# Performance work log

Hardware: AMD Instinct MI355X
Metric: run time of the kernel (lower is better)

## Reference

```python
import jax, jax.numpy as jnp
import numpy as np

B, Q, K, C, H = 4, 1024, 1024, 1024, 16
L = C            # latent_dim (== in_dim per module construction)
CH = L // H      # head_dim = 64


def _ln(x, w, b):
    m = jnp.mean(x, -1, keepdims=True)
    v = jnp.mean((x - m) ** 2, -1, keepdims=True)
    return (x - m) * jax.lax.rsqrt(v + 1e-5) * w + b


def setup_inputs() -> dict:
    key = jax.random.key(0)
    ks = jax.random.split(key, 16)
    s = 0.02
    return {
        "queries": jax.random.normal(ks[0], (B, Q, C), jnp.float32),
        "contexts": jax.random.normal(ks[1], (B, K, C), jnp.float32),
        "queries_hidden": jax.random.normal(ks[2], (B, Q, L), jnp.float32),
        "sa_norm_w": jnp.ones((C,), jnp.float32),
        "sa_norm_b": jnp.zeros((C,), jnp.float32),
        "sa_qkv_w": jax.random.normal(ks[3], (C, 2 * L + C), jnp.float32) * s,
        "sa_out_w": jax.random.normal(ks[4], (C, C), jnp.float32) * s,
        "sa_out_b": jnp.zeros((C,), jnp.float32),
        "ca_norm_w": jnp.ones((C,), jnp.float32),
        "ca_norm_b": jnp.zeros((C,), jnp.float32),
        "gru_w_ih": jax.random.normal(ks[5], (3 * L, C), jnp.float32) * s,
        "gru_w_hh": jax.random.normal(ks[6], (3 * L, L), jnp.float32) * s,
        "gru_b_ih": jnp.zeros((3 * L,), jnp.float32),
        "gru_b_hh": jnp.zeros((3 * L,), jnp.float32),
        "ca_k_w": jax.random.normal(ks[7], (C, L), jnp.float32) * s,
        "ca_v_w": jax.random.normal(ks[8], (C, C), jnp.float32) * s,
        "ca_out_w": jax.random.normal(ks[9], (C, C), jnp.float32) * s,
        "ca_out_b": jnp.zeros((C,), jnp.float32),
        "ln1_w": jnp.ones((C,), jnp.float32),
        "ln1_b": jnp.zeros((C,), jnp.float32),
        "lin1_w": jax.random.normal(ks[10], (C, 2 * C), jnp.float32) * s,
        "ln2_w": jnp.ones((2 * C,), jnp.float32),
        "ln2_b": jnp.zeros((2 * C,), jnp.float32),
        "lin2_w": jax.random.normal(ks[11], (2 * C, C), jnp.float32) * s,
    }


def reference(queries, contexts, queries_hidden,
              sa_norm_w, sa_norm_b, sa_qkv_w, sa_out_w, sa_out_b,
              ca_norm_w, ca_norm_b, gru_w_ih, gru_w_hh, gru_b_ih, gru_b_hh,
              ca_k_w, ca_v_w, ca_out_w, ca_out_b,
              ln1_w, ln1_b, lin1_w, ln2_w, ln2_b, lin2_w):
    scale = 1.0 / jnp.sqrt(jnp.asarray(C, queries.dtype))

    # ---- SelfAttention (pre-norm, residual) ----
    xn = _ln(queries, sa_norm_w, sa_norm_b)
    qkv = (xn @ sa_qkv_w).reshape(B, Q, H, -1)          # [B,Q,H, 2*CH + C/H]
    q, k, v = jnp.split(qkv, [CH, 2 * CH], axis=-1)
    e = jnp.einsum('nqhc,nkhc->nhqk', q, k) * scale
    a = jax.nn.softmax(e, axis=-1)
    o = jnp.einsum('nhqk,nkhc->nqhc', a, v).reshape(B, Q, C)
    x = o @ sa_out_w + sa_out_b + queries

    # ---- AttentionDynamicQuery (GRU-updated queries, cross-attn) ----
    x_pre = x
    xn = _ln(x, ca_norm_w, ca_norm_b)
    xf = xn.reshape(B * Q, C)
    hf = queries_hidden.reshape(B * Q, L)
    gi = xf @ gru_w_ih.T + gru_b_ih                     # [BQ, 3L]
    gh = hf @ gru_w_hh.T + gru_b_hh
    gir, giz, gin = jnp.split(gi, 3, axis=-1)
    ghr, ghz, ghn = jnp.split(gh, 3, axis=-1)
    r = jax.nn.sigmoid(gir + ghr)
    z = jax.nn.sigmoid(giz + ghz)
    n = jnp.tanh(gin + r * ghn)
    h = (1.0 - z) * n + z * hf                          # PyTorch GRUCell update
    qh = h.reshape(B, Q, H, CH)                         # new queries_hidden

    kk = (contexts @ ca_k_w).reshape(B, K, H, CH)
    vv = (contexts @ ca_v_w).reshape(B, K, H, C // H)
    energy = jnp.einsum('nqhc,nkhc->nhqk', qh, kk)      # returned UNscaled
    att = jax.nn.softmax(energy * scale, axis=-1)
    o = jnp.einsum('nhqk,nkhc->nqhc', att, vv).reshape(B, Q, C)
    x = o @ ca_out_w + ca_out_b + x_pre

    # ---- MLP: LN -> SiLU -> Linear -> LN -> SiLU -> Linear, residual ----
    m = jax.nn.silu(_ln(x, ln1_w, ln1_b)) @ lin1_w
    m = jax.nn.silu(_ln(m, ln2_w, ln2_b)) @ lin2_w
    out = x + m                                         # dropout(p=0) = identity
    return (out, energy, qh)
```

## Files before the change

### kernel.cpp

```cpp
#include <hip/hip_runtime.h>
#include <hip/hip_bf16.h>
#include <math.h>

static constexpr float SCALE = 0.03125f;

typedef __attribute__((ext_vector_type(4))) float f32x4;
typedef __attribute__((ext_vector_type(8))) __bf16 bf16x8;
typedef __attribute__((ext_vector_type(4))) __bf16 bf16x4;

__device__ __forceinline__ void g2l16(const void* g, void* l) {
  __builtin_amdgcn_global_load_lds(
      (const __attribute__((address_space(1))) unsigned int*)g,
      (__attribute__((address_space(3))) unsigned int*)l,
      16, 0, 0);
}

__global__ __launch_bounds__(256) void prep_all(
    const float* __restrict__ sa_qkv_w, const float* __restrict__ ca_k_w,
    const float* __restrict__ ca_v_w, const float* __restrict__ sa_out_w,
    const float* __restrict__ ca_out_w, const float* __restrict__ lin1_w,
    const float* __restrict__ lin2_w, const float* __restrict__ gru_w_ih,
    const float* __restrict__ gru_w_hh, const float* __restrict__ qhid,
    const float* __restrict__ contexts,
    const float* __restrict__ queries, const float* __restrict__ sa_norm_w,
    const float* __restrict__ sa_norm_b,
    __bf16* __restrict__ qkvT, __bf16* __restrict__ kT, __bf16* __restrict__ vT,
    __bf16* __restrict__ saoT, __bf16* __restrict__ caoT, __bf16* __restrict__ lin1T,
    __bf16* __restrict__ lin2T, __bf16* __restrict__ ihB, __bf16* __restrict__ hhB,
    __bf16* __restrict__ qhB, __bf16* __restrict__ ctxB, __bf16* __restrict__ xnB) {
  int bid = blockIdx.x;
  int t = threadIdx.x;
  if (bid >= 9984) {
    int row = bid - 9984;
    int c = t * 4;
    float4 v = *(const float4*)(queries + (size_t)row * 1024 + c);
    float s = v.x + v.y + v.z + v.w;
    float s2 = v.x*v.x + v.y*v.y + v.z*v.z + v.w*v.w;
    #pragma unroll
    for (int off = 32; off > 0; off >>= 1) {
      s += __shfl_xor(s, off);
      s2 += __shfl_xor(s2, off);
    }
    __shared__ float red[4], red2[4];
    int wv = t >> 6;
    if ((t & 63) == 0) { red[wv] = s; red2[wv] = s2; }
    __syncthreads();
    float S  = red[0] + red[1] + red[2] + red[3];
    float S2 = red2[0] + red2[1] + red2[2] + red2[3];
    float mean = S / 1024.f;
    float var = S2 / 1024.f - mean * mean;
    float rs = rsqrtf(var + 1e-5f);
    float vv[4] = {v.x, v.y, v.z, v.w};
    bf16x4 o;
    #pragma unroll
    for (int j = 0; j < 4; ++j)
      o[j] = (__bf16)((vv[j] - mean) * rs * sa_norm_w[c+j] + sa_norm_b[c+j]);
    *(bf16x4*)(xnB + (size_t)row * 1024 + c) = o;
    return;
  }
  if (bid >= 2816) {
    const float* csrc; __bf16* cdst; int cbase;
    if (bid < 4352)      { csrc = gru_w_ih; cdst = ihB;  cbase = 2816; }
    else if (bid < 5888) { csrc = gru_w_hh; cdst = hhB;  cbase = 4352; }
    else if (bid < 7936) { csrc = qhid;     cdst = qhB;  cbase = 5888; }
    else                 { csrc = contexts; cdst = ctxB; cbase = 7936; }
    size_t idx = ((size_t)(bid - cbase) * 256 + t) * 8;
    float4 a = *(const float4*)(csrc + idx);
    float4 b = *(const float4*)(csrc + idx + 4);
    bf16x8 o = {(__bf16)a.x,(__bf16)a.y,(__bf16)a.z,(__bf16)a.w,
                (__bf16)b.x,(__bf16)b.y,(__bf16)b.z,(__bf16)b.w};
    *(bf16x8*)(cdst + idx) = o;
    return;
  }
  const float* src; __bf16* dst; int Kd, N, base;
  if (bid < 768)       { src = sa_qkv_w; dst = qkvT;  Kd = 1024; N = 3072; base = 0; }
  else if (bid < 1024) { src = ca_k_w;   dst = kT;    Kd = 1024; N = 1024; base = 768; }
  else if (bid < 1280) { src = ca_v_w;   dst = vT;    Kd = 1024; N = 1024; base = 1024; }
  else if (bid < 1536) { src = sa_out_w; dst = saoT;  Kd = 1024; N = 1024; base = 1280; }
  else if (bid < 1792) { src = ca_out_w; dst = caoT;  Kd = 1024; N = 1024; base = 1536; }
  else if (bid < 2304) { src = lin1_w;   dst = lin1T; Kd = 1024; N = 2048; base = 1792; }
  else                 { src = lin2_w;   dst = lin2T; Kd = 2048; N = 1024; base = 2304; }
  int tid = bid - base;
  int ntx = N >> 6;
  int n0 = (tid % ntx) * 64, k0 = (tid / ntx) * 64;
  __shared__ float tile[64][65];
  #pragma unroll
  for (int i = 0; i < 16; ++i) {
    int idx = i * 256 + t; int r = idx >> 6, c = idx & 63;
    tile[r][c] = src[(size_t)(k0 + r) * N + n0 + c];
  }
  __syncthreads();
  #pragma unroll
  for (int i = 0; i < 16; ++i) {
    int idx = i * 256 + t; int r = idx >> 6, c = idx & 63;
    dst[(size_t)(n0 + r) * Kd + k0 + c] = (__bf16)tile[c][r];
  }
}

template <int NV>
__global__ __launch_bounds__(256) void ln_bf16(
    const float* __restrict__ xf, const __bf16* __restrict__ xb,
    const float* __restrict__ w, const float* __restrict__ b,
    __bf16* __restrict__ out, int silu) {
  const int D = NV * 1024;
  int row = blockIdx.x, t = threadIdx.x;
  float vals[NV * 4];
  float s = 0.f, s2 = 0.f;
  #pragma unroll
  for (int i = 0; i < NV; ++i) {
    int c = (i * 256 + t) * 4;
    float4 v;
    if (xf) {
      v = *(const float4*)(xf + (size_t)row * D + c);
    } else {
      bf16x4 vb = *(const bf16x4*)(xb + (size_t)row * D + c);
      v = make_float4((float)vb[0], (float)vb[1], (float)vb[2], (float)vb[3]);
    }
    vals[i*4+0] = v.x; vals[i*4+1] = v.y; vals[i*4+2] = v.z; vals[i*4+3] = v.w;
    s += v.x + v.y + v.z + v.w;
    s2 += v.x*v.x + v.y*v.y + v.z*v.z + v.w*v.w;
  }
  #pragma unroll
  for (int off = 32; off > 0; off >>= 1) {
    s += __shfl_xor(s, off);
    s2 += __shfl_xor(s2, off);
  }
  __shared__ float red[4], red2[4];
  int wv = t >> 6;
  if ((t & 63) == 0) { red[wv] = s; red2[wv] = s2; }
  __syncthreads();
  float S  = red[0] + red[1] + red[2] + red[3];
  float S2 = red2[0] + red2[1] + red2[2] + red2[3];
  float mean = S / D;
  float var = S2 / D - mean * mean;
  float rs = rsqrtf(var + 1e-5f);
  #pragma unroll
  for (int i = 0; i < NV; ++i) {
    int c = (i * 256 + t) * 4;
    bf16x4 o;
    #pragma unroll
    for (int j = 0; j < 4; ++j) {
      float v = (vals[i*4+j] - mean) * rs * w[c+j] + b[c+j];
      if (silu) v = v / (1.f + __expf(-v));
      o[j] = (__bf16)v;
    }
    *(bf16x4*)(out + (size_t)row * D + c) = o;
  }
}

__device__ __forceinline__ void gemm_body(
    const __bf16* __restrict__ A, long long lda,
    const __bf16* __restrict__ B, long long ldb,
    float* __restrict__ outF, __bf16* __restrict__ outB, long long ldc,
    const float* __restrict__ bias, const float* __restrict__ res,
    int K, int bm, int bn, __bf16* __restrict__ VTout, int vmode) {
  __shared__ __bf16 Asm0[8192];
  __shared__ __bf16 Bsm0[8192];
  __shared__ __bf16 Asm1[8192];
  __shared__ __bf16 Bsm1[8192];
  int t = threadIdx.x;
  int lane = t & 63, w = t >> 6;
  int l15 = lane & 15, kg = lane >> 4;
  int wm = (w >> 1) * 64, wn = (w & 1) * 64;

  f32x4 acc[4][4];
  #pragma unroll
  for (int i = 0; i < 4; ++i)
    #pragma unroll
    for (int j = 0; j < 4; ++j) acc[i][j] = (f32x4)(0.0f);

  const __bf16* ga[4]; const __bf16* gb[4];
  int lo[4];
  #pragma unroll
  for (int i = 0; i < 4; ++i) {
    int slot = i * 256 + t;
    int row = slot >> 3, s = slot & 7;
    int sx = s ^ (row & 7);
    ga[i] = A + (size_t)(bm + row) * lda + (sx << 3);
    gb[i] = B + (size_t)(bn + row) * ldb + (sx << 3);
    lo[i] = (i * 256 + w * 64) << 3;
  }

  auto STAGE = [&](__bf16* As, __bf16* Bs, int k0) {
    #pragma unroll
    for (int i = 0; i < 4; ++i) g2l16(ga[i] + k0, As + lo[i]);
    #pragma unroll
    for (int i = 0; i < 4; ++i) g2l16(gb[i] + k0, Bs + lo[i]);
  };
  auto COMPUTE = [&](const __bf16* As, const __bf16* Bs) {
    #pragma unroll
    for (int kk = 0; kk < 2; ++kk) {
      bf16x8 af[4], bfr[4];
      #pragma unroll
      for (int mi = 0; mi < 4; ++mi) {
        int row = wm + mi * 16 + l15;
        int ks = kk * 4 + kg;
        af[mi] = *(const bf16x8*)(As + row * 64 + ((ks ^ (row & 7)) << 3));
      }
      #pragma unroll
      for (int ni = 0; ni < 4; ++ni) {
        int row = wn + ni * 16 + l15;
        int ks = kk * 4 + kg;
        bfr[ni] = *(const bf16x8*)(Bs + row * 64 + ((ks ^ (row & 7)) << 3));
      }
      #pragma unroll
      for (int mi = 0; mi < 4; ++mi)
        #pragma unroll
        for (int ni = 0; ni < 4; ++ni)
          acc[mi][ni] = __builtin_amdgcn_mfma_f32_16x16x32_bf16(
              af[mi], bfr[ni], acc[mi][ni], 0, 0, 0);
    }
  };
  #define GEMM_SYNC() do { \
    asm volatile("s_waitcnt vmcnt(0)" ::: "memory"); \
    __builtin_amdgcn_s_barrier(); \
    __builtin_amdgcn_sched_barrier(0); \
  } while (0)

  STAGE(Asm0, Bsm0, 0);
  GEMM_SYNC();
  int nk = K >> 6;
  for (int kt = 0; kt + 2 < nk; kt += 2) {
    STAGE(Asm1, Bsm1, (kt + 1) << 6);
    COMPUTE(Asm0, Bsm0);
    GEMM_SYNC();
    STAGE(Asm0, Bsm0, (kt + 2) << 6);
    COMPUTE(Asm1, Bsm1);
    GEMM_SYNC();
  }
  STAGE(Asm1, Bsm1, (nk - 1) << 6);
  COMPUTE(Asm0, Bsm0);
  GEMM_SYNC();
  COMPUTE(Asm1, Bsm1);
  #undef GEMM_SYNC

  int cw = bn + wn;
  int isV = 0;
  if (vmode == 1)      isV = (cw % 192) == 128;
  else if (vmode == 2) isV = cw >= 1024;

  if (isV) {
    int h = (vmode == 1) ? (cw / 192) : ((cw - 1024) >> 6);
    int rowb = bm + wm;
    int b = rowb >> 10, k0 = rowb & 1023;
    __bf16* scr = (w < 2 ? Asm0 : Bsm0) + (w & 1) * 4096;
    #pragma unroll
    for (int mi = 0; mi < 4; ++mi) {
      #pragma unroll
      for (int ni = 0; ni < 4; ++ni) {
        int d = ni * 16 + l15;
        int sw = (d & 7) << 3;
        #pragma unroll
        for (int r = 0; r < 4; ++r) {
          int kl = mi * 16 + kg * 4 + r;
          scr[d * 64 + (kl ^ sw)] = (__bf16)acc[mi][ni][r];
        }
      }
    }
    #pragma unroll
    for (int i = 0; i < 8; ++i) {
      int idx = i * 64 + lane;
      int d = idx >> 3, kc = (idx & 7) * 8;
      bf16x8 v = *(const bf16x8*)&scr[d * 64 + (kc ^ ((d & 7) << 3))];
      *(bf16x8*)(VTout + ((size_t)((b * 16 + h) * 64 + d) << 10) + k0 + kc) = v;
    }
    return;
  }

  #pragma unroll
  for (int mi = 0; mi < 4; ++mi) {
    #pragma unroll
    for (int ni = 0; ni < 4; ++ni) {
      int rbase = bm + wm + mi * 16 + kg * 4;
      int c = bn + wn + ni * 16 + l15;
      #pragma unroll
      for (int r = 0; r < 4; ++r) {
        float val = acc[mi][ni][r];
        if (bias) val += bias[c];
        size_t off = (size_t)(rbase + r) * ldc + c;
        if (res) val += res[off];
        if (outF) outF[off] = val;
        if (outB) outB[off] = (__bf16)val;
      }
    }
  }
}

__global__ __launch_bounds__(256) void gemm_bf16(
    const __bf16* __restrict__ A, long long lda,
    const __bf16* __restrict__ B, long long ldb,
    float* __restrict__ outF, __bf16* __restrict__ outB, long long ldc,
    const float* __restrict__ bias, const float* __restrict__ res, int K,
    __bf16* __restrict__ VTout, int vmode) {
  int nwg = gridDim.x * gridDim.y;
  int orig = blockIdx.y * gridDim.x + blockIdx.x;
  int swz = (orig & 7) * (nwg >> 3) + (orig >> 3);
  gemm_body(A, lda, B, ldb, outF, outB, ldc, bias, res, K,
            (swz / gridDim.x) * 128, (swz % gridDim.x) * 128, VTout, vmode);
}

__global__ __launch_bounds__(256) void gemm_dual(
    const __bf16* __restrict__ A0, long long lda0, const __bf16* __restrict__ B0, long long ldb0,
    float* __restrict__ oF0, __bf16* __restrict__ oB0, long long ldc0,
    const float* __restrict__ bias0, const float* __restrict__ res0, int K0, int gx0, int nb0,
    const __bf16* __restrict__ A1, long long lda1, const __bf16* __restrict__ B1, long long ldb1,
    float* __restrict__ oF1, __bf16* __restrict__ oB1, long long ldc1,
    const float* __restrict__ bias1, const float* __restrict__ res1, int K1, int gx1,
    __bf16* __restrict__ VT1, int vm1) {
  int bid = blockIdx.x;
  if (bid < nb0) {
    int swz = (bid & 7) * (nb0 >> 3) + (bid >> 3);
    gemm_body(A0, lda0, B0, ldb0, oF0, oB0, ldc0, bias0, res0, K0,
              (swz / gx0) * 128, (swz % gx0) * 128, nullptr, 0);
  } else {
    int b = bid - nb0;
    int nb1 = gridDim.x - nb0;
    int swz = (b & 7) * (nb1 >> 3) + (b >> 3);
    gemm_body(A1, lda1, B1, ldb1, oF1, oB1, ldc1, bias1, res1, K1,
              (swz / gx1) * 128, (swz % gx1) * 128, VT1, vm1);
  }
}

__global__ __launch_bounds__(256) void gru_kernel(
    const __bf16* __restrict__ gi, const __bf16* __restrict__ gh,
    const float* __restrict__ hf, float* __restrict__ qh, __bf16* __restrict__ qhb) {
  size_t e0 = ((size_t)blockIdx.x * 256 + threadIdx.x) * 8;
  int row = (int)(e0 >> 10), col = (int)(e0 & 1023);
  size_t base = (size_t)row * 3072 + col;
  bf16x8 vir = *(const bf16x8*)(gi + base);
  bf16x8 viz = *(const bf16x8*)(gi + base + 1024);
  bf16x8 vin = *(const bf16x8*)(gi + base + 2048);
  bf16x8 vhr = *(const bf16x8*)(gh + base);
  bf16x8 vhz = *(const bf16x8*)(gh + base + 1024);
  bf16x8 vhn = *(const bf16x8*)(gh + base + 2048);
  float4 h0 = *(const float4*)(hf + e0);
  float4 h1 = *(const float4*)(hf + e0 + 4);
  float hv[8] = {h0.x, h0.y, h0.z, h0.w, h1.x, h1.y, h1.z, h1.w};
  float q[8];
  #pragma unroll
  for (int j = 0; j < 8; ++j) {
    float r = 1.f / (1.f + __expf(-((float)vir[j] + (float)vhr[j])));
    float z = 1.f / (1.f + __expf(-((float)viz[j] + (float)vhz[j])));
    float n = tanhf((float)vin[j] + r * (float)vhn[j]);
    q[j] = (1.f - z) * n + z * hv[j];
  }
  *(float4*)(qh + e0)     = make_float4(q[0], q[1], q[2], q[3]);
  *(float4*)(qh + e0 + 4) = make_float4(q[4], q[5], q[6], q[7]);
  bf16x8 qb;
  #pragma unroll
  for (int j = 0; j < 8; ++j) qb[j] = (__bf16)q[j];
  *(bf16x8*)(qhb + e0) = qb;
}

template <int E>
__global__ __launch_bounds__(256) void flash_attn(
    const __bf16* __restrict__ Qb, long long q_sb, long long q_sh, int q_sm,
    const __bf16* __restrict__ Kb, long long k_sb, long long k_sh, int k_sm,
    const __bf16* __restrict__ VT, __bf16* __restrict__ Ob,
    float* __restrict__ energyOut, float scale) {
  __shared__ __bf16 Ksm[3][4096];
  __shared__ __bf16 Vsm[3][4096];
  __shared__ __bf16 Psm[128 * 64];
  __shared__ float corr_l[128];
  __shared__ float l_l[128];
  int g = blockIdx.y, b = g >> 4, h = g & 15;
  int qt = blockIdx.x * 128;
  const __bf16* Qg = Qb + (size_t)b * q_sb + (size_t)h * q_sh;
  const __bf16* Kg = Kb + (size_t)b * k_sb + (size_t)h * k_sh;
  const __bf16* Vg = VT + (size_t)g * 65536;
  int t = threadIdx.x, lane = t & 63, w = t >> 6;
  int l15 = lane & 15, kg = lane >> 4;
  int wq = w * 32;

  bf16x8 qf[2][2];
  #pragma unroll
  for (int nq = 0; nq < 2; ++nq)
    #pragma unroll
    for (int kk = 0; kk < 2; ++kk)
      qf[nq][kk] = *(const bf16x8*)(
          Qg + (size_t)(qt + wq + nq * 16 + l15) * q_sm + kk * 32 + kg * 8);

  f32x4 acc_o[2][4];
  #pragma unroll
  for (int i = 0; i < 2; ++i)
    #pragma unroll
    for (int j = 0; j < 4; ++j) acc_o[i][j] = (f32x4)(0.0f);
  float m_run[2] = {-1e30f, -1e30f};
  float l_run[2] = {0.f, 0.f};

  const __bf16* gK[2]; const __bf16* gV[2];
  int lo[2];
  #pragma unroll
  for (int i = 0; i < 2; ++i) {
    int slot = i * 256 + t;
    int row = slot >> 3, s = slot & 7, sx = s ^ (row & 7);
    gK[i] = Kg + (size_t)row * k_sm + (sx << 3);
    gV[i] = Vg + (size_t)row * 1024 + (sx << 3);
    lo[i] = (i * 256 + w * 64) << 3;
  }

  #pragma unroll
  for (int i = 0; i < 2; ++i) g2l16(gK[i], &Ksm[0][lo[i]]);
  #pragma unroll
  for (int i = 0; i < 2; ++i) g2l16(gV[i], &Vsm[0][lo[i]]);
  #pragma unroll
  for (int i = 0; i < 2; ++i) g2l16(gK[i] + (size_t)64 * k_sm, &Ksm[1][lo[i]]);
  #pragma unroll
  for (int i = 0; i < 2; ++i) g2l16(gV[i] + 64, &Vsm[1][lo[i]]);

  int rb = 0;
  for (int kvt = 0; kvt < 16; ++kvt) {
    if (E) {
      if (kvt == 0)       asm volatile("s_waitcnt vmcnt(4)" ::: "memory");
      else if (kvt == 1)  asm volatile("s_waitcnt vmcnt(12)" ::: "memory");
      else if (kvt == 15) asm volatile("s_waitcnt vmcnt(16)" ::: "memory");
      else                asm volatile("s_waitcnt vmcnt(20)" ::: "memory");
    } else {
      if (kvt == 15)      asm volatile("s_waitcnt vmcnt(0)" ::: "memory");
      else                asm volatile("s_waitcnt vmcnt(4)" ::: "memory");
    }
    __builtin_amdgcn_s_barrier();
    __builtin_amdgcn_sched_barrier(0);

    if (kvt < 14) {
      int sbuf = rb >= 1 ? rb - 1 : rb + 2;
      size_t ko = (size_t)(kvt + 2) << 6;
      #pragma unroll
      for (int i = 0; i < 2; ++i) g2l16(gK[i] + ko * k_sm, &Ksm[sbuf][lo[i]]);
      #pragma unroll
      for (int i = 0; i < 2; ++i) g2l16(gV[i] + ko, &Vsm[sbuf][lo[i]]);
    }
    const __bf16* Ks = Ksm[rb];
    const __bf16* Vs = Vsm[rb];

    f32x4 accs[4][2];
    #pragma unroll
    for (int i = 0; i < 4; ++i)
      #pragma unroll
      for (int j = 0; j < 2; ++j) accs[i][j] = (f32x4)(0.0f);
    __builtin_amdgcn_s_setprio(1);
    #pragma unroll
    for (int tt = 0; tt < 4; ++tt) {
      bf16x8 kf[2];
      #pragma unroll
      for (int kk = 0; kk < 2; ++kk) {
        int row = tt * 16 + l15;
        int ks = kk * 4 + kg;
        kf[kk] = *(const bf16x8*)(Ks + row * 64 + ((ks ^ (row & 7)) << 3));
      }
      #pragma unroll
      for (int nq = 0; nq < 2; ++nq)
        #pragma unroll
        for (int kk = 0; kk < 2; ++kk)
          accs[tt][nq] = __builtin_amdgcn_mfma_f32_16x16x32_bf16(
              kf[kk], qf[nq][kk], accs[tt][nq], 0, 0, 0);
    }
    __builtin_amdgcn_s_setprio(0);

    if (E) {
      int kv0 = kvt << 6;
      float* eg = energyOut + ((size_t)g << 20);
      #pragma unroll
      for (int nq = 0; nq < 2; ++nq) {
        int q = qt + wq + nq * 16 + l15;
        #pragma unroll
        for (int tt = 0; tt < 4; ++tt)
          __builtin_nontemporal_store(
              accs[tt][nq], (f32x4*)(eg + (size_t)q * 1024 + kv0 + tt * 16 + kg * 4));
      }
    }

    #pragma unroll
    for (int nq = 0; nq < 2; ++nq) {
      float tmax = -1e30f;
      #pragma unroll
      for (int tt = 0; tt < 4; ++tt)
        #pragma unroll
        for (int r = 0; r < 4; ++r) tmax = fmaxf(tmax, accs[tt][nq][r]);
      tmax *= scale;
      tmax = fmaxf(tmax, __shfl_xor(tmax, 16));
      tmax = fmaxf(tmax, __shfl_xor(tmax, 32));
      float m_new = fmaxf(m_run[nq], tmax);
      float corr = __expf(m_run[nq] - m_new);
      m_run[nq] = m_new;
      int q = wq + nq * 16 + l15;
      float psum = 0.f;
      #pragma unroll
      for (int tt = 0; tt < 4; ++tt) {
        bf16x4 p4;
        #pragma unroll
        for (int r = 0; r < 4; ++r) {
          float p = __expf(accs[tt][nq][r] * scale - m_new);
          psum += p;
          p4[r] = (__bf16)p;
        }
        int kvs = (tt * 16 + kg * 4) ^ ((q & 7) << 3);
        *(bf16x4*)(Psm + q * 64 + kvs) = p4;
      }
      psum += __shfl_xor(psum, 16);
      psum += __shfl_xor(psum, 32);
      l_run[nq] = l_run[nq] * corr + psum;
      if (kg == 0) corr_l[q] = corr;
    }

    #pragma unroll
    for (int mq = 0; mq < 2; ++mq) {
      f32x4 c4 = *(const f32x4*)&corr_l[wq + mq * 16 + kg * 4];
      #pragma unroll
      for (int nd = 0; nd < 4; ++nd)
        #pragma unroll
        for (int r = 0; r < 4; ++r) acc_o[mq][nd][r] *= c4[r];
    }
    __builtin_amdgcn_s_setprio(1);
    #pragma unroll
    for (int kk = 0; kk < 2; ++kk) {
      bf16x8 pf[2], vf[4];
      #pragma unroll
      for (int mq = 0; mq < 2; ++mq) {
        int row = wq + mq * 16 + l15;
        int kvs = (kk * 32 + kg * 8) ^ ((row & 7) << 3);
        pf[mq] = *(const bf16x8*)(Psm + row * 64 + kvs);
      }
      #pragma unroll
      for (int nd = 0; nd < 4; ++nd) {
        int vrow = nd * 16 + l15;
        vf[nd] = *(const bf16x8*)(Vs + vrow * 64 + (((kk * 4 + kg) ^ (vrow & 7)) << 3));
      }
      #pragma unroll
      for (int mq = 0; mq < 2; ++mq)
        #pragma unroll
        for (int nd = 0; nd < 4; ++nd)
          acc_o[mq][nd] = __builtin_amdgcn_mfma_f32_16x16x32_bf16(
              pf[mq], vf[nd], acc_o[mq][nd], 0, 0, 0);
    }
    __builtin_amdgcn_s_setprio(0);
    rb = rb == 2 ? 0 : rb + 1;
  }

  #pragma unroll
  for (int nq = 0; nq < 2; ++nq)
    if (kg == 0) l_l[wq + nq * 16 + l15] = l_run[nq];
  __syncthreads();

  #pragma unroll
  for (int mq = 0; mq < 2; ++mq) {
    f32x4 lv = *(const f32x4*)&l_l[wq + mq * 16 + kg * 4];
    #pragma unroll
    for (int nd = 0; nd < 4; ++nd) {
      int col = h * 64 + nd * 16 + l15;
      #pragma unroll
      for (int r = 0; r < 4; ++r) {
        int qrow = qt + wq + mq * 16 + kg * 4 + r;
        Ob[(size_t)(b * 1024 + qrow) * 1024 + col] = (__bf16)(acc_o[mq][nd][r] / lv[r]);
      }
    }
  }
}

extern "C" void kernel_launch(void* const* d_in, const int* in_sizes, int n_in,
                              void* d_out, int out_size, void* d_ws, size_t ws_size,
                              hipStream_t stream) {
  (void)in_sizes; (void)n_in; (void)out_size; (void)ws_size;
  const float* queries   = (const float*)d_in[0];
  const float* contexts  = (const float*)d_in[1];
  const float* qhid      = (const float*)d_in[2];
  const float* sa_norm_w = (const float*)d_in[3];
  const float* sa_norm_b = (const float*)d_in[4];
  const float* sa_qkv_w  = (const float*)d_in[5];
  const float* sa_out_w  = (const float*)d_in[6];
  const float* sa_out_b  = (const float*)d_in[7];
  const float* ca_norm_w = (const float*)d_in[8];
  const float* ca_norm_b = (const float*)d_in[9];
  const float* gru_w_ih  = (const float*)d_in[10];
  const float* gru_w_hh  = (const float*)d_in[11];
  const float* gru_b_ih  = (const float*)d_in[12];
  const float* gru_b_hh  = (const float*)d_in[13];
  const float* ca_k_w    = (const float*)d_in[14];
  const float* ca_v_w    = (const float*)d_in[15];
  const float* ca_out_w  = (const float*)d_in[16];
  const float* ca_out_b  = (const float*)d_in[17];
  const float* ln1_w     = (const float*)d_in[18];
  const float* ln1_b     = (const float*)d_in[19];
  const float* lin1_w    = (const float*)d_in[20];
  const float* ln2_w     = (const float*)d_in[21];
  const float* ln2_b     = (const float*)d_in[22];
  const float* lin2_w    = (const float*)d_in[23];

  float* out0   = (float*)d_out;
  float* energy = out0 + (size_t)4194304;
  float* qh_out = out0 + (size_t)71303168;

  const size_t MM = 1u << 20;
  float* ws = (float*)d_ws;
  float*  X     = ws;
  float*  X2    = ws + 4 * MM;
  __bf16* M1B    = (__bf16*)(ws + 9 * MM);
  __bf16* XN_b   = (__bf16*)(ws + 17 * MM);
  __bf16* QHID_b = (__bf16*)(ws + 19 * MM);
  __bf16* CTX_b  = (__bf16*)(ws + 21 * MM);
  __bf16* O_b    = (__bf16*)(ws + 23 * MM);
  __bf16* VT_b   = (__bf16*)(ws + 25 * MM);
  __bf16* QKV_b  = (__bf16*)(ws + 27 * MM);
  __bf16* KV_b   = (__bf16*)(ws + 27 * MM);
  __bf16* LN2_b  = (__bf16*)(ws);
  __bf16* qkvT   = (__bf16*)(ws + 33 * MM);
  __bf16* ihB    = (__bf16*)(ws + 34 * MM + MM / 2);
  __bf16* hhB    = (__bf16*)(ws + 36 * MM);
  __bf16* kT     = (__bf16*)(ws + 37 * MM + MM / 2);
  __bf16* vT     = (__bf16*)(ws + 38 * MM);
  __bf16* saoT   = (__bf16*)(ws + 38 * MM + MM / 2);
  __bf16* caoT   = (__bf16*)(ws + 39 * MM);
  __bf16* lin1T  = (__bf16*)(ws + 39 * MM + MM / 2);
  __bf16* lin2T  = (__bf16*)(ws + 40 * MM + MM / 2);
  __bf16* GI_b = (__bf16*)energy;
  __bf16* GH_b = (__bf16*)(energy + 6 * MM);

  const long long QKV_SB = 1024LL * 3072;
  const long long KV_SB  = 1024LL * 2048;

  prep_all<<<14080, 256, 0, stream>>>(
      sa_qkv_w, ca_k_w, ca_v_w, sa_out_w, ca_out_w, lin1_w, lin2_w,
      gru_w_ih, gru_w_hh, qhid, contexts, queries, sa_norm_w, sa_norm_b,
      qkvT, kT, vT, saoT, caoT, lin1T, lin2T, ihB, hhB, QHID_b, CTX_b, XN_b);

  gemm_bf16<<<dim3(24, 32), 256, 0, stream>>>(
      XN_b, 1024, qkvT, 1024, nullptr, QKV_b, 3072, nullptr, nullptr, 1024, VT_b, 1);
  flash_attn<0><<<dim3(8, 64), 256, 0, stream>>>(
      QKV_b, QKV_SB, 192, 3072, QKV_b + 64, QKV_SB, 192, 3072,
      VT_b, O_b, nullptr, SCALE);
  gemm_dual<<<1024, 256, 0, stream>>>(
      O_b, 1024, saoT, 1024, X, nullptr, 1024, sa_out_b, queries, 1024, 8, 256,
      QHID_b, 1024, hhB, 1024, nullptr, GH_b, 3072, gru_b_hh, nullptr, 1024, 24,
      nullptr, 0);

  ln_bf16<1><<<4096, 256, 0, stream>>>(X, nullptr, ca_norm_w, ca_norm_b, XN_b, 0);
  gemm_dual<<<1280, 256, 0, stream>>>(
      XN_b, 1024, ihB, 1024, nullptr, GI_b, 3072, gru_b_ih, nullptr, 1024, 24, 768,
      CTX_b, 1024, kT, 1024, nullptr, KV_b, 2048, nullptr, nullptr, 1024, 16,
      VT_b, 2);
  gru_kernel<<<2048, 256, 0, stream>>>(GI_b, GH_b, qhid, qh_out, QHID_b );

  flash_attn<1><<<dim3(8, 64), 256, 0, stream>>>(
      QHID_b, 1024LL * 1024, 64, 1024, KV_b, KV_SB, 64, 2048,
      VT_b, O_b, energy, SCALE);
  gemm_bf16<<<dim3(8, 32), 256, 0, stream>>>(
      O_b, 1024, caoT, 1024, X2, nullptr, 1024, ca_out_b, X, 1024, nullptr, 0);

  ln_bf16<1><<<4096, 256, 0, stream>>>(X2, nullptr, ln1_w, ln1_b, XN_b, 1);
  gemm_bf16<<<dim3(16, 32), 256, 0, stream>>>(
      XN_b, 1024, lin1T, 1024, nullptr, M1B, 2048, nullptr, nullptr, 1024, nullptr, 0);
  ln_bf16<2><<<4096, 256, 0, stream>>>(nullptr, M1B, ln2_w, ln2_b, LN2_b, 1);
  gemm_bf16<<<dim3(8, 32), 256, 0, stream>>>(
      LN2_b, 2048, lin2T, 2048, out0, nullptr, 1024, nullptr, X2, 2048, nullptr, 0);
}
```

Measured before the change: 609.5 us.

## Split prep into critical path and fuse remaining conversions into QKV GEMM launch

The prep work is split in two. A small kernel now transposes only the QKV weight and computes the first LayerNorm. The remaining weight transposes and bf16 casts run as extra blocks inside the same launch as the QKV projection GEMM, so that memory-bound conversion work can overlap with the compute-bound GEMM instead of preceding it. Shared memory is now a single buffer passed into gemm_body so it can be reused by the transpose tiles. The cost is that the merged launch uses the larger GEMM shared-memory footprint for every block, including the transpose blocks.

```diff
diff --git a/kernel.cpp b/kernel.cpp
--- a/kernel.cpp
+++ b/kernel.cpp
@@ -15,47 +15,310 @@
       16, 0, 0);
 }
 
-__global__ __launch_bounds__(256) void prep_all(
-    const float* __restrict__ sa_qkv_w, const float* __restrict__ ca_k_w,
-    const float* __restrict__ ca_v_w, const float* __restrict__ sa_out_w,
-    const float* __restrict__ ca_out_w, const float* __restrict__ lin1_w,
-    const float* __restrict__ lin2_w, const float* __restrict__ gru_w_ih,
-    const float* __restrict__ gru_w_hh, const float* __restrict__ qhid,
-    const float* __restrict__ contexts,
+__device__ __forceinline__ void wtrans_tile(
+    const float* __restrict__ src, __bf16* __restrict__ dst,
+    int Kd, int N, int tid, float (*tile)[65]) {
+  int t = threadIdx.x;
+  int ntx = N >> 6;
+  int n0 = (tid % ntx) * 64, k0 = (tid / ntx) * 64;
+  #pragma unroll
+  for (int i = 0; i < 16; ++i) {
+    int idx = i * 256 + t; int r = idx >> 6, c = idx & 63;
+    tile[r][c] = src[(size_t)(k0 + r) * N + n0 + c];
+  }
+  __syncthreads();
+  #pragma unroll
+  for (int i = 0; i < 16; ++i) {
+    int idx = i * 256 + t; int r = idx >> 6, c = idx & 63;
+    dst[(size_t)(n0 + r) * Kd + k0 + c] = (__bf16)tile[c][r];
+  }
+}
+
+__global__ __launch_bounds__(256) void prep_crit(
+    const float* __restrict__ sa_qkv_w,
     const float* __restrict__ queries, const float* __restrict__ sa_norm_w,
     const float* __restrict__ sa_norm_b,
-    __bf16* __restrict__ qkvT, __bf16* __restrict__ kT, __bf16* __restrict__ vT,
-    __bf16* __restrict__ saoT, __bf16* __restrict__ caoT, __bf16* __restrict__ lin1T,
-    __bf16* __restrict__ lin2T, __bf16* __restrict__ ihB, __bf16* __restrict__ hhB,
-    __bf16* __restrict__ qhB, __bf16* __restrict__ ctxB, __bf16* __restrict__ xnB) {
+    __bf16* __restrict__ qkvT, __bf16* __restrict__ xnB) {
   int bid = blockIdx.x;
   int t = threadIdx.x;
-  if (bid >= 9984) {
-    int row = bid - 9984;
-    int c = t * 4;
-    float4 v = *(const float4*)(queries + (size_t)row * 1024 + c);
-    float s = v.x + v.y + v.z + v.w;
-    float s2 = v.x*v.x + v.y*v.y + v.z*v.z + v.w*v.w;
-    #pragma unroll
-    for (int off = 32; off > 0; off >>= 1) {
-      s += __shfl_xor(s, off);
-      s2 += __shfl_xor(s2, off);
-    }
-    __shared__ float red[4], red2[4];
-    int wv = t >> 6;
-    if ((t & 63) == 0) { red[wv] = s; red2[wv] = s2; }
-    __syncthreads();
-    float S  = red[0] + red[1] + red[2] + red[3];
-    float S2 = red2[0] + red2[1] + red2[2] + red2[3];
-    float mean = S / 1024.f;
-    float var = S2 / 1024.f - mean * mean;
-    float rs = rsqrtf(var + 1e-5f);
-    float vv[4] = {v.x, v.y, v.z, v.w};
+  if (bid < 768) {
+    __shared__ float tile[64][65];
+    wtrans_tile(sa_qkv_w, qkvT, 1024, 3072, bid, tile);
+    return;
+  }
+  int row = bid - 768;
+  int c = t * 4;
+  float4 v = *(const float4*)(queries + (size_t)row * 1024 + c);
+  float s = v.x + v.y + v.z + v.w;
+  float s2 = v.x*v.x + v.y*v.y + v.z*v.z + v.w*v.w;
+  #pragma unroll
+  for (int off = 32; off > 0; off >>= 1) {
+    s += __shfl_xor(s, off);
+    s2 += __shfl_xor(s2, off);
+  }
+  __shared__ float red[4], red2[4];
+  int wv = t >> 6;
+  if ((t & 63) == 0) { red[wv] = s; red2[wv] = s2; }
+  __syncthreads();
+  float S  = red[0] + red[1] + red[2] + red[3];
+  float S2 = red2[0] + red2[1] + red2[2] + red2[3];
+  float mean = S / 1024.f;
+  float var = S2 / 1024.f - mean * mean;
+  float rs = rsqrtf(var + 1e-5f);
+  float vv[4] = {v.x, v.y, v.z, v.w};
+  bf16x4 o;
+  #pragma unroll
+  for (int j = 0; j < 4; ++j)
+    o[j] = (__bf16)((vv[j] - mean) * rs * sa_norm_w[c+j] + sa_norm_b[c+j]);
+  *(bf16x4*)(xnB + (size_t)row * 1024 + c) = o;
+}
+
+template <int NV>
+__global__ __launch_bounds__(256) void ln_bf16(
+    const float* __restrict__ xf, const __bf16* __restrict__ xb,
+    const float* __restrict__ w, const float* __restrict__ b,
+    __bf16* __restrict__ out, int silu) {
+  const int D = NV * 1024;
+  int row = blockIdx.x, t = threadIdx.x;
+  float vals[NV * 4];
+  float s = 0.f, s2 = 0.f;
+  #pragma unroll
+  for (int i = 0; i < NV; ++i) {
+    int c = (i * 256 + t) * 4;
+    float4 v;
+    if (xf) {
+      v = *(const float4*)(xf + (size_t)row * D + c);
+    } else {
+      bf16x4 vb = *(const bf16x4*)(xb + (size_t)row * D + c);
+      v = make_float4((float)vb[0], (float)vb[1], (float)vb[2], (float)vb[3]);
+    }
+    vals[i*4+0] = v.x; vals[i*4+1] = v.y; vals[i*4+2] = v.z; vals[i*4+3] = v.w;
+    s += v.x + v.y + v.z + v.w;
+    s2 += v.x*v.x + v.y*v.y + v.z*v.z + v.w*v.w;
+  }
+  #pragma unroll
+  for (int off = 32; off > 0; off >>= 1) {
+    s += __shfl_xor(s, off);
+    s2 += __shfl_xor(s2, off);
+  }
+  __shared__ float red[4], red2[4];
+  int wv = t >> 6;
+  if ((t & 63) == 0) { red[wv] = s; red2[wv] = s2; }
+  __syncthreads();
+  float S  = red[0] + red[1] + red[2] + red[3];
+  float S2 = red2[0] + red2[1] + red2[2] + red2[3];
+  float mean = S / D;
+  float var = S2 / D - mean * mean;
+  float rs = rsqrtf(var + 1e-5f);
+  #pragma unroll
+  for (int i = 0; i < NV; ++i) {
+    int c = (i * 256 + t) * 4;
     bf16x4 o;
     #pragma unroll
-    for (int j = 0; j < 4; ++j)
-      o[j] = (__bf16)((vv[j] - mean) * rs * sa_norm_w[c+j] + sa_norm_b[c+j]);
-    *(bf16x4*)(xnB + (size_t)row * 1024 + c) = o;
+    for (int j = 0; j < 4; ++j) {
+      float v = (vals[i*4+j] - mean) * rs * w[c+j] + b[c+j];
+      if (silu) v = v / (1.f + __expf(-v));
+      o[j] = (__bf16)v;
+    }
+    *(bf16x4*)(out + (size_t)row * D + c) = o;
+  }
+}
+
+__device__ __forceinline__ void gemm_body(
+    __bf16* __restrict__ sm,
+    const __bf16* __restrict__ A, long long lda,
+    const __bf16* __restrict__ B, long long ldb,
+    float* __restrict__ outF, __bf16* __restrict__ outB, long long ldc,
+    const float* __restrict__ bias, const float* __restrict__ res,
+    int K, int bm, int bn, __bf16* __restrict__ VTout, int vmode) {
+  __bf16* Asm0 = sm;
+  __bf16* Bsm0 = sm + 8192;
+  __bf16* Asm1 = sm + 16384;
+  __bf16* Bsm1 = sm + 24576;
+  int t = threadIdx.x;
+  int lane = t & 63, w = t >> 6;
+  int l15 = lane & 15, kg = lane >> 4;
+  int wm = (w >> 1) * 64, wn = (w & 1) * 64;
+
+  f32x4 acc[4][4];
+  #pragma unroll
+  for (int i = 0; i < 4; ++i)
+    #pragma unroll
+    for (int j = 0; j < 4; ++j) acc[i][j] = (f32x4)(0.0f);
+
+  const __bf16* ga[4]; const __bf16* gb[4];
+  int lo[4];
+  #pragma unroll
+  for (int i = 0; i < 4; ++i) {
+    int slot = i * 256 + t;
+    int row = slot >> 3, s = slot & 7;
+    int sx = s ^ (row & 7);
+    ga[i] = A + (size_t)(bm + row) * lda + (sx << 3);
+    gb[i] = B + (size_t)(bn + row) * ldb + (sx << 3);
+    lo[i] = (i * 256 + w * 64) << 3;
+  }
+
+  auto STAGE = [&](__bf16* As, __bf16* Bs, int k0) {
+    #pragma unroll
+    for (int i = 0; i < 4; ++i) g2l16(ga[i] + k0, As + lo[i]);
+    #pragma unroll
+    for (int i = 0; i < 4; ++i) g2l16(gb[i] + k0, Bs + lo[i]);
+  };
+  auto COMPUTE = [&](const __bf16* As, const __bf16* Bs) {
+    #pragma unroll
+    for (int kk = 0; kk < 2; ++kk) {
+      bf16x8 af[4], bfr[4];
+      #pragma unroll
+      for (int mi = 0; mi < 4; ++mi) {
+        int row = wm + mi * 16 + l15;
+        int ks = kk * 4 + kg;
+        af[mi] = *(const bf16x8*)(As + row * 64 + ((ks ^ (row & 7)) << 3));
+      }
+      #pragma unroll
+      for (int ni = 0; ni < 4; ++ni) {
+        int row = wn + ni * 16 + l15;
+        int ks = kk * 4 + kg;
+        bfr[ni] = *(const bf16x8*)(Bs + row * 64 + ((ks ^ (row & 7)) << 3));
+      }
+      #pragma unroll
+      for (int mi = 0; mi < 4; ++mi)
+        #pragma unroll
+        for (int ni = 0; ni < 4; ++ni)
+          acc[mi][ni] = __builtin_amdgcn_mfma_f32_16x16x32_bf16(
+              af[mi], bfr[ni], acc[mi][ni], 0, 0, 0);
+    }
+  };
+  #define GEMM_SYNC() do { \
+    asm volatile("s_waitcnt vmcnt(0)" ::: "memory"); \
+    __builtin_amdgcn_s_barrier(); \
+    __builtin_amdgcn_sched_barrier(0); \
+  } while (0)
+
+  STAGE(Asm0, Bsm0, 0);
+  GEMM_SYNC();
+  int nk = K >> 6;
+  for (int kt = 0; kt + 2 < nk; kt += 2) {
+    STAGE(Asm1, Bsm1, (kt + 1) << 6);
+    COMPUTE(Asm0, Bsm0);
+    GEMM_SYNC();
+    STAGE(Asm0, Bsm0, (kt + 2) << 6);
+    COMPUTE(Asm1, Bsm1);
+    GEMM_SYNC();
+  }
+  STAGE(Asm1, Bsm1, (nk - 1) << 6);
+  COMPUTE(Asm0, Bsm0);
+  GEMM_SYNC();
+  COMPUTE(Asm1, Bsm1);
+  #undef GEMM_SYNC
+
+  int cw = bn + wn;
+  int isV = 0;
+  if (vmode == 1)      isV = (cw % 192) == 128;
+  else if (vmode == 2) isV = cw >= 1024;
+
+  if (isV) {
+    int h = (vmode == 1) ? (cw / 192) : ((cw - 1024) >> 6);
+    int rowb = bm + wm;
+    int b = rowb >> 10, k0 = rowb & 1023;
+    __bf16* scr = (w < 2 ? Asm0 : Bsm0) + (w & 1) * 4096;
+    #pragma unroll
+    for (int mi = 0; mi < 4; ++mi) {
+      #pragma unroll
+      for (int ni = 0; ni < 4; ++ni) {
+        int d = ni * 16 + l15;
+        int sw = (d & 7) << 3;
+        #pragma unroll
+        for (int r = 0; r < 4; ++r) {
+          int kl = mi * 16 + kg * 4 + r;
+          scr[d * 64 + (kl ^ sw)] = (__bf16)acc[mi][ni][r];
+        }
+      }
+    }
+    #pragma unroll
+    for (int i = 0; i < 8; ++i) {
+      int idx = i * 64 + lane;
+      int d = idx >> 3, kc = (idx & 7) * 8;
+      bf16x8 v = *(const bf16x8*)&scr[d * 64 + (kc ^ ((d & 7) << 3))];
+      *(bf16x8*)(VTout + ((size_t)((b * 16 + h) * 64 + d) << 10) + k0 + kc) = v;
+    }
+    return;
+  }
+
+  #pragma unroll
+  for (int mi = 0; mi < 4; ++mi) {
+    #pragma unroll
+    for (int ni = 0; ni < 4; ++ni) {
+      int rbase = bm + wm + mi * 16 + kg * 4;
+      int c = bn + wn + ni * 16 + l15;
+      #pragma unroll
+      for (int r = 0; r < 4; ++r) {
+        float val = acc[mi][ni][r];
+        if (bias) val += bias[c];
+        size_t off = (size_t)(rbase + r) * ldc + c;
+        if (res) val += res[off];
+        if (outF) outF[off] = val;
+        if (outB) outB[off] = (__bf16)val;
+      }
+    }
+  }
+}
+
+__global__ __launch_bounds__(256) void gemm_bf16(
+    const __bf16* __restrict__ A, long long lda,
+    const __bf16* __restrict__ B, long long ldb,
+    float* __restrict__ outF, __bf16* __restrict__ outB, long long ldc,
+    const float* __restrict__ bias, const float* __restrict__ res, int K,
+    __bf16* __restrict__ VTout, int vmode) {
+  __shared__ __bf16 sm[32768];
+  int nwg = gridDim.x * gridDim.y;
+  int orig = blockIdx.y * gridDim.x + blockIdx.x;
+  int swz = (orig & 7) * (nwg >> 3) + (orig >> 3);
+  gemm_body(sm, A, lda, B, ldb, outF, outB, ldc, bias, res, K,
+            (swz / gridDim.x) * 128, (swz % gridDim.x) * 128, VTout, vmode);
+}
+
+__global__ __launch_bounds__(256) void gemm_dual(
+    const __bf16* __restrict__ A0, long long lda0, const __bf16* __restrict__ B0, long long ldb0,
+    float* __restrict__ oF0, __bf16* __restrict__ oB0, long long ldc0,
+    const float* __restrict__ bias0, const float* __restrict__ res0, int K0, int gx0, int nb0,
+    const __bf16* __restrict__ A1, long long lda1, const __bf16* __restrict__ B1, long long ldb1,
+    float* __restrict__ oF1, __bf16* __restrict__ oB1, long long ldc1,
+    const float* __restrict__ bias1, const float* __restrict__ res1, int K1, int gx1,
+    __bf16* __restrict__ VT1, int vm1) {
+  __shared__ __bf16 sm[32768];
+  int bid = blockIdx.x;
+  if (bid < nb0) {
+    int swz = (bid & 7) * (nb0 >> 3) + (bid >> 3);
+    gemm_body(sm, A0, lda0, B0, ldb0, oF0, oB0, ldc0, bias0, res0, K0,
+              (swz / gx0) * 128, (swz % gx0) * 128, nullptr, 0);
+  } else {
+    int b = bid - nb0;
+    int nb1 = gridDim.x - nb0;
+    int swz = (b & 7) * (nb1 >> 3) + (b >> 3);
+    gemm_body(sm, A1, lda1, B1, ldb1, oF1, oB1, ldc1, bias1, res1, K1,
+              (swz / gx1) * 128, (swz % gx1) * 128, VT1, vm1);
+  }
+}
+
+__global__ __launch_bounds__(256) void gemm_prep(
+    const __bf16* __restrict__ Aq, const __bf16* __restrict__ Bq,
+    __bf16* __restrict__ Cq, __bf16* __restrict__ VTq,
+    const float* __restrict__ ca_k_w, const float* __restrict__ ca_v_w,
+    const float* __restrict__ sa_out_w, const float* __restrict__ ca_out_w,
+    const float* __restrict__ lin1_w, const float* __restrict__ lin2_w,
+    const float* __restrict__ gru_w_ih, const float* __restrict__ gru_w_hh,
+    const float* __restrict__ qhid, const float* __restrict__ contexts,
+    __bf16* __restrict__ kT, __bf16* __restrict__ vT, __bf16* __restrict__ saoT,
+    __bf16* __restrict__ caoT, __bf16* __restrict__ lin1T, __bf16* __restrict__ lin2T,
+    __bf16* __restrict__ ihB, __bf16* __restrict__ hhB,
+    __bf16* __restrict__ qhB, __bf16* __restrict__ ctxB) {
+  __shared__ __bf16 sm[32768];
+  int bid = blockIdx.x;
+  int t = threadIdx.x;
+  if (bid < 768) {
+    int swz = (bid & 7) * 96 + (bid >> 3);
+    gemm_body(sm, Aq, 1024, Bq, 1024, nullptr, Cq, 3072, nullptr, nullptr, 1024,
+              (swz / 24) * 128, (swz % 24) * 128, VTq, 1);
     return;
   }
   if (bid >= 2816) {
@@ -73,252 +336,13 @@
     return;
   }
   const float* src; __bf16* dst; int Kd, N, base;
-  if (bid < 768)       { src = sa_qkv_w; dst = qkvT;  Kd = 1024; N = 3072; base = 0; }
-  else if (bid < 1024) { src = ca_k_w;   dst = kT;    Kd = 1024; N = 1024; base = 768; }
+  if (bid < 1024)      { src = ca_k_w;   dst = kT;    Kd = 1024; N = 1024; base = 768; }
   else if (bid < 1280) { src = ca_v_w;   dst = vT;    Kd = 1024; N = 1024; base = 1024; }
   else if (bid < 1536) { src = sa_out_w; dst = saoT;  Kd = 1024; N = 1024; base = 1280; }
   else if (bid < 1792) { src = ca_out_w; dst = caoT;  Kd = 1024; N = 1024; base = 1536; }
   else if (bid < 2304) { src = lin1_w;   dst = lin1T; Kd = 1024; N = 2048; base = 1792; }
   else                 { src = lin2_w;   dst = lin2T; Kd = 2048; N = 1024; base = 2304; }
-  int tid = bid - base;
-  int ntx = N >> 6;
-  int n0 = (tid % ntx) * 64, k0 = (tid / ntx) * 64;
-  __shared__ float tile[64][65];
-  #pragma unroll
-  for (int i = 0; i < 16; ++i) {
-    int idx = i * 256 + t; int r = idx >> 6, c = idx & 63;
-    tile[r][c] = src[(size_t)(k0 + r) * N + n0 + c];
-  }
-  __syncthreads();
-  #pragma unroll
-  for (int i = 0; i < 16; ++i) {
-    int idx = i * 256 + t; int r = idx >> 6, c = idx & 63;
-    dst[(size_t)(n0 + r) * Kd + k0 + c] = (__bf16)tile[c][r];
-  }
-}
-
-template <int NV>
-__global__ __launch_bounds__(256) void ln_bf16(
-    const float* __restrict__ xf, const __bf16* __restrict__ xb,
-    const float* __restrict__ w, const float* __restrict__ b,
-    __bf16* __restrict__ out, int silu) {
-  const int D = NV * 1024;
-  int row = blockIdx.x, t = threadIdx.x;
-  float vals[NV * 4];
-  float s = 0.f, s2 = 0.f;
-  #pragma unroll
-  for (int i = 0; i < NV; ++i) {
-    int c = (i * 256 + t) * 4;
-    float4 v;
-    if (xf) {
-      v = *(const float4*)(xf + (size_t)row * D + c);
-    } else {
-      bf16x4 vb = *(const bf16x4*)(xb + (size_t)row * D + c);
-      v = make_float4((float)vb[0], (float)vb[1], (float)vb[2], (float)vb[3]);
-    }
-    vals[i*4+0] = v.x; vals[i*4+1] = v.y; vals[i*4+2] = v.z; vals[i*4+3] = v.w;
-    s += v.x + v.y + v.z + v.w;
-    s2 += v.x*v.x + v.y*v.y + v.z*v.z + v.w*v.w;
-  }
-  #pragma unroll
-  for (int off = 32; off > 0; off >>= 1) {
-    s += __shfl_xor(s, off);
-    s2 += __shfl_xor(s2, off);
-  }
-  __shared__ float red[4], red2[4];
-  int wv = t >> 6;
-  if ((t & 63) == 0) { red[wv] = s; red2[wv] = s2; }
-  __syncthreads();
-  float S  = red[0] + red[1] + red[2] + red[3];
-  float S2 = red2[0] + red2[1] + red2[2] + red2[3];
-  float mean = S / D;
-  float var = S2 / D - mean * mean;
-  float rs = rsqrtf(var + 1e-5f);
-  #pragma unroll
-  for (int i = 0; i < NV; ++i) {
-    int c = (i * 256 + t) * 4;
-    bf16x4 o;
-    #pragma unroll
-    for (int j = 0; j < 4; ++j) {
-      float v = (vals[i*4+j] - mean) * rs * w[c+j] + b[c+j];
-      if (silu) v = v / (1.f + __expf(-v));
-      o[j] = (__bf16)v;
-    }
-    *(bf16x4*)(out + (size_t)row * D + c) = o;
-  }
-}
-
-__device__ __forceinline__ void gemm_body(
-    const __bf16* __restrict__ A, long long lda,
-    const __bf16* __restrict__ B, long long ldb,
-    float* __restrict__ outF, __bf16* __restrict__ outB, long long ldc,
-    const float* __restrict__ bias, const float* __restrict__ res,
-    int K, int bm, int bn, __bf16* __restrict__ VTout, int vmode) {
-  __shared__ __bf16 Asm0[8192];
-  __shared__ __bf16 Bsm0[8192];
-  __shared__ __bf16 Asm1[8192];
-  __shared__ __bf16 Bsm1[8192];
-  int t = threadIdx.x;
-  int lane = t & 63, w = t >> 6;
-  int l15 = lane & 15, kg = lane >> 4;
-  int wm = (w >> 1) * 64, wn = (w & 1) * 64;
-
-  f32x4 acc[4][4];
-  #pragma unroll
-  for (int i = 0; i < 4; ++i)
-    #pragma unroll
-    for (int j = 0; j < 4; ++j) acc[i][j] = (f32x4)(0.0f);
-
-  const __bf16* ga[4]; const __bf16* gb[4];
-  int lo[4];
-  #pragma unroll
-  for (int i = 0; i < 4; ++i) {
-    int slot = i * 256 + t;
-    int row = slot >> 3, s = slot & 7;
-    int sx = s ^ (row & 7);
-    ga[i] = A + (size_t)(bm + row) * lda + (sx << 3);
-    gb[i] = B + (size_t)(bn + row) * ldb + (sx << 3);
-    lo[i] = (i * 256 + w * 64) << 3;
-  }
-
-  auto STAGE = [&](__bf16* As, __bf16* Bs, int k0) {
-    #pragma unroll
-    for (int i = 0; i < 4; ++i) g2l16(ga[i] + k0, As + lo[i]);
-    #pragma unroll
-    for (int i = 0; i < 4; ++i) g2l16(gb[i] + k0, Bs + lo[i]);
-  };
-  auto COMPUTE = [&](const __bf16* As, const __bf16* Bs) {
-    #pragma unroll
-    for (int kk = 0; kk < 2; ++kk) {
-      bf16x8 af[4], bfr[4];
-      #pragma unroll
-      for (int mi = 0; mi < 4; ++mi) {
-        int row = wm + mi * 16 + l15;
-        int ks = kk * 4 + kg;
-        af[mi] = *(const bf16x8*)(As + row * 64 + ((ks ^ (row & 7)) << 3));
-      }
-      #pragma unroll
-      for (int ni = 0; ni < 4; ++ni) {
-        int row = wn + ni * 16 + l15;
-        int ks = kk * 4 + kg;
-        bfr[ni] = *(const bf16x8*)(Bs + row * 64 + ((ks ^ (row & 7)) << 3));
-      }
-      #pragma unroll
-      for (int mi = 0; mi < 4; ++mi)
-        #pragma unroll
-        for (int ni = 0; ni < 4; ++ni)
-          acc[mi][ni] = __builtin_amdgcn_mfma_f32_16x16x32_bf16(
-              af[mi], bfr[ni], acc[mi][ni], 0, 0, 0);
-    }
-  };
-  #define GEMM_SYNC() do { \
-    asm volatile("s_waitcnt vmcnt(0)" ::: "memory"); \
-    __builtin_amdgcn_s_barrier(); \
-    __builtin_amdgcn_sched_barrier(0); \
-  } while (0)
-
-  STAGE(Asm0, Bsm0, 0);
-  GEMM_SYNC();
-  int nk = K >> 6;
-  for (int kt = 0; kt + 2 < nk; kt += 2) {
-    STAGE(Asm1, Bsm1, (kt + 1) << 6);
-    COMPUTE(Asm0, Bsm0);
-    GEMM_SYNC();
-    STAGE(Asm0, Bsm0, (kt + 2) << 6);
-    COMPUTE(Asm1, Bsm1);
-    GEMM_SYNC();
-  }
-  STAGE(Asm1, Bsm1, (nk - 1) << 6);
-  COMPUTE(Asm0, Bsm0);
-  GEMM_SYNC();
-  COMPUTE(Asm1, Bsm1);
-  #undef GEMM_SYNC
-
-  int cw = bn + wn;
-  int isV = 0;
-  if (vmode == 1)      isV = (cw % 192) == 128;
-  else if (vmode == 2) isV = cw >= 1024;
-
-  if (isV) {
-    int h = (vmode == 1) ? (cw / 192) : ((cw - 1024) >> 6);
-    int rowb = bm + wm;
-    int b = rowb >> 10, k0 = rowb & 1023;
-    __bf16* scr = (w < 2 ? Asm0 : Bsm0) + (w & 1) * 4096;
-    #pragma unroll
-    for (int mi = 0; mi < 4; ++mi) {
-      #pragma unroll
-      for (int ni = 0; ni < 4; ++ni) {
-        int d = ni * 16 + l15;
-        int sw = (d & 7) << 3;
-        #pragma unroll
-        for (int r = 0; r < 4; ++r) {
-          int kl = mi * 16 + kg * 4 + r;
-          scr[d * 64 + (kl ^ sw)] = (__bf16)acc[mi][ni][r];
-        }
-      }
-    }
-    #pragma unroll
-    for (int i = 0; i < 8; ++i) {
-      int idx = i * 64 + lane;
-      int d = idx >> 3, kc = (idx & 7) * 8;
-      bf16x8 v = *(const bf16x8*)&scr[d * 64 + (kc ^ ((d & 7) << 3))];
-      *(bf16x8*)(VTout + ((size_t)((b * 16 + h) * 64 + d) << 10) + k0 + kc) = v;
-    }
-    return;
-  }
-
-  #pragma unroll
-  for (int mi = 0; mi < 4; ++mi) {
-    #pragma unroll
-    for (int ni = 0; ni < 4; ++ni) {
-      int rbase = bm + wm + mi * 16 + kg * 4;
-      int c = bn + wn + ni * 16 + l15;
-      #pragma unroll
-      for (int r = 0; r < 4; ++r) {
-        float val = acc[mi][ni][r];
-        if (bias) val += bias[c];
-        size_t off = (size_t)(rbase + r) * ldc + c;
-        if (res) val += res[off];
-        if (outF) outF[off] = val;
-        if (outB) outB[off] = (__bf16)val;
-      }
-    }
-  }
-}
-
-__global__ __launch_bounds__(256) void gemm_bf16(
-    const __bf16* __restrict__ A, long long lda,
-    const __bf16* __restrict__ B, long long ldb,
-    float* __restrict__ outF, __bf16* __restrict__ outB, long long ldc,
-    const float* __restrict__ bias, const float* __restrict__ res, int K,
-    __bf16* __restrict__ VTout, int vmode) {
-  int nwg = gridDim.x * gridDim.y;
-  int orig = blockIdx.y * gridDim.x + blockIdx.x;
-  int swz = (orig & 7) * (nwg >> 3) + (orig >> 3);
-  gemm_body(A, lda, B, ldb, outF, outB, ldc, bias, res, K,
-            (swz / gridDim.x) * 128, (swz % gridDim.x) * 128, VTout, vmode);
-}
-
-__global__ __launch_bounds__(256) void gemm_dual(
-    const __bf16* __restrict__ A0, long long lda0, const __bf16* __restrict__ B0, long long ldb0,
-    float* __restrict__ oF0, __bf16* __restrict__ oB0, long long ldc0,
-    const float* __restrict__ bias0, const float* __restrict__ res0, int K0, int gx0, int nb0,
-    const __bf16* __restrict__ A1, long long lda1, const __bf16* __restrict__ B1, long long ldb1,
-    float* __restrict__ oF1, __bf16* __restrict__ oB1, long long ldc1,
-    const float* __restrict__ bias1, const float* __restrict__ res1, int K1, int gx1,
-    __bf16* __restrict__ VT1, int vm1) {
-  int bid = blockIdx.x;
-  if (bid < nb0) {
-    int swz = (bid & 7) * (nb0 >> 3) + (bid >> 3);
-    gemm_body(A0, lda0, B0, ldb0, oF0, oB0, ldc0, bias0, res0, K0,
-              (swz / gx0) * 128, (swz % gx0) * 128, nullptr, 0);
-  } else {
-    int b = bid - nb0;
-    int nb1 = gridDim.x - nb0;
-    int swz = (b & 7) * (nb1 >> 3) + (b >> 3);
-    gemm_body(A1, lda1, B1, ldb1, oF1, oB1, ldc1, bias1, res1, K1,
-              (swz / gx1) * 128, (swz % gx1) * 128, VT1, vm1);
-  }
+  wtrans_tile(src, dst, Kd, N, bid - base, (float(*)[65])sm);
 }
 
 __global__ __launch_bounds__(256) void gru_kernel(
@@ -618,13 +642,14 @@
   const long long QKV_SB = 1024LL * 3072;
   const long long KV_SB  = 1024LL * 2048;
 
-  prep_all<<<14080, 256, 0, stream>>>(
-      sa_qkv_w, ca_k_w, ca_v_w, sa_out_w, ca_out_w, lin1_w, lin2_w,
-      gru_w_ih, gru_w_hh, qhid, contexts, queries, sa_norm_w, sa_norm_b,
-      qkvT, kT, vT, saoT, caoT, lin1T, lin2T, ihB, hhB, QHID_b, CTX_b, XN_b);
-
-  gemm_bf16<<<dim3(24, 32), 256, 0, stream>>>(
-      XN_b, 1024, qkvT, 1024, nullptr, QKV_b, 3072, nullptr, nullptr, 1024, VT_b, 1);
+  prep_crit<<<4864, 256, 0, stream>>>(
+      sa_qkv_w, queries, sa_norm_w, sa_norm_b, qkvT, XN_b);
+
+  gemm_prep<<<9984, 256, 0, stream>>>(
+      XN_b, qkvT, QKV_b, VT_b,
+      ca_k_w, ca_v_w, sa_out_w, ca_out_w, lin1_w, lin2_w,
+      gru_w_ih, gru_w_hh, qhid, contexts,
+      kT, vT, saoT, caoT, lin1T, lin2T, ihB, hhB, QHID_b, CTX_b);
   flash_attn<0><<<dim3(8, 64), 256, 0, stream>>>(
       QKV_b, QKV_SB, 192, 3072, QKV_b + 64, QKV_SB, 192, 3072,
       VT_b, O_b, nullptr, SCALE);
```

Result: faster. 591.0 us (-3.0%).
